# Kernel tuning notes

Hardware: AMD Instinct MI355X
Metric: run time of the kernel (lower is better)

Reference implementation:

```python
import jax, jax.numpy as jnp
import numpy as np

LEN_NOISE = 1000
LEN_INTERVAL_U = 50
INPUT_DIM = 3
OUTPUT_DIM = 3
HIDDEN_DIM = 512
LOGSIG_CH = INPUT_DIM + (INPUT_DIM * (INPUT_DIM - 1)) // 2  # depth-2 Lyndon basis: level1 + Levy area


def _static_schedule(window_size):
    """Replicates compute_multilevel_logsignature index logic + the u_logsigrnn
    pop-gating of the forward loop. All quantities are static given window_size."""
    tb = np.linspace(0.0, 1.0, LEN_NOISE)
    tu = tb[::LEN_INTERVAL_U]
    tt = np.linspace(0.0, 1.0, window_size)
    u_indices = np.searchsorted(tb, tu, side='right') - 1
    t_indices = np.searchsorted(tb, tt[1:], side='right') - 1
    u_idx_for_t = np.searchsorted(tu, tt[1:], side='right') - 1
    starts, ends, u_times, last = [], [], [], -1
    for it, iu in zip(t_indices, u_idx_for_t):
        iu = max(int(iu), 0)
        if iu != last:
            u_times.append(float(tu[iu]))
            last = iu
        starts.append(int(u_indices[iu]))
        ends.append(int(it))
    u_times.append(float(tt[-1]))
    gates, q = [], list(u_times)
    for t in tt:  # gate True -> last_h updated to h at this step
        if q and t >= q[0]:
            q.pop(0)
            gates.append(True)
        else:
            gates.append(False)
    return np.array(starts), np.array(ends), np.array(gates)


def _logsig_depth2(path, starts, ends):
    """Depth-2 log-signature (Lyndon basis) of path[:, starts[k]:ends[k]+1] with
    basepoint=True. Level-1 = endpoint (basepoint is 0); level-2 = Levy area,
    computed from a cumulative cross-product prefix sum (basepoint segment
    0 -> path[:,start] contributes zero area)."""
    cross = 0.5 * (path[:, :-1, :, None] * path[:, 1:, None, :]
                   - path[:, :-1, None, :] * path[:, 1:, :, None])  # [B,L-1,d,d]
    C = jnp.cumsum(cross, axis=1)
    C = jnp.concatenate([jnp.zeros_like(C[:, :1]), C], axis=1)      # [B,L,d,d]
    lvl1 = path[:, ends]                                            # [B,T-1,d]
    area = C[:, ends] - C[:, starts]                                # [B,T-1,d,d]
    iu, ju = np.triu_indices(path.shape[-1], k=1)
    return jnp.concatenate([lvl1, area[:, :, iu, ju]], axis=-1)     # [B,T-1,d+C(d,2)]


def setup_inputs() -> dict:
    key = jax.random.key(0)
    ks = jax.random.split(key, 8)
    B, W = 1024, 64
    in_rnn = HIDDEN_DIM + LOGSIG_CH

    def kaiming(k, shape):
        return jax.random.normal(k, shape, jnp.float32) * np.float32(np.sqrt(2.0 / shape[1]))

    return {
        "z": jax.random.normal(ks[0], (B, LEN_NOISE, INPUT_DIM), jnp.float32),
        "W1": kaiming(ks[1], (HIDDEN_DIM, in_rnn)),
        "b1": jnp.zeros((HIDDEN_DIM,), jnp.float32),
        "W2": kaiming(ks[2], (HIDDEN_DIM, HIDDEN_DIM)),
        "b2": jnp.zeros((HIDDEN_DIM,), jnp.float32),
        "W3": kaiming(ks[3], (HIDDEN_DIM, HIDDEN_DIM)),
        "b3": jnp.zeros((HIDDEN_DIM,), jnp.float32),
        "Wout": kaiming(ks[4], (OUTPUT_DIM, HIDDEN_DIM)),
        "batch_size": B,
        "window_size": W,
    }


def reference(z, W1, b1, W2, b2, W3, b3, Wout, batch_size, window_size):
    starts, ends, gates = _static_schedule(window_size)
    # Brownian path: z[:,0]=0, z[:,1:] *= sqrt(dt), cumsum
    dt = 1.0 / (LEN_NOISE - 1)
    zz = z.at[:, 0].set(0.0)
    zz = zz.at[:, 1:].multiply(np.float32(np.sqrt(dt)))
    bp = jnp.cumsum(zz, axis=1)                                     # [B,L,d]
    ls = _logsig_depth2(bp, starts, ends)                           # [B,T-1,ch]
    ls = jnp.concatenate([jnp.zeros_like(ls[:, :1]), ls], axis=1)   # [B,T,ch] (zero prepended)

    def mlp(x):  # FeedForwardNN([h,h]) + Tanh
        h = jax.nn.relu(x @ W1.T + b1)
        h = jax.nn.relu(h @ W2.T + b2)
        return jnp.tanh(h @ W3.T + b3)

    h0 = jnp.zeros((z.shape[0], HIDDEN_DIM), z.dtype)  # init_fixed=True

    def step(last_h, inp):
        ls_t, gate = inp
        h = mlp(jnp.concatenate([last_h, ls_t], axis=-1))
        out = h @ Wout.T  # linear, no bias
        return jnp.where(gate, h, last_h), out

    xs = (jnp.swapaxes(ls, 0, 1), jnp.asarray(gates))
    _, outs = jax.lax.scan(step, h0, xs)                            # [T,B,out]
    return jnp.swapaxes(outs, 0, 1)                                 # [B,T,out]
```

## Files before the change

kernel.cpp:

```cpp
#include <hip/hip_runtime.h>
#include <cmath>

#define WIN 64
#define HID 512
#define BATCH 1024
#define KIN 518

typedef _Float16 f16;
typedef _Float16 half8 __attribute__((ext_vector_type(8)));
typedef float f32x4 __attribute__((ext_vector_type(4)));
typedef unsigned short u16x4 __attribute__((ext_vector_type(4)));

struct Sched { int starts[63]; int ends[63]; };
struct TL { int t[8]; int gf[8]; };
struct Targ { int v[32]; };

__global__ __launch_bounds__(256)
void logsig_scan(const float* __restrict__ z, Sched sc,
                 ushort* __restrict__ lsh, float scale) {
  __shared__ float zs[3000];
  __shared__ float Cs[20][3];
  __shared__ float wtot[4][6];
  __shared__ float earr[63][6];
  __shared__ short fe_s[1000];
  const int tid = threadIdx.x;
  const int b = blockIdx.x;
  const int ln = tid & 63, wv = tid >> 6;

  const float4* zrow = (const float4*)(z + (size_t)b * 3000);
  for (int i = tid; i < 750; i += 256) ((float4*)zs)[i] = zrow[i];
  for (int i = tid; i < 1000; i += 256) fe_s[i] = -1;
  if (tid == 0) { Cs[0][0] = 0.f; Cs[0][1] = 0.f; Cs[0][2] = 0.f; }
  __syncthreads();
  if (tid < 63) fe_s[sc.ends[tid]] = (short)tid;
  __syncthreads();

  const int p0 = 4 * tid + 1;
  int myfe[4];
#pragma unroll
  for (int i = 0; i < 4; ++i) myfe[i] = (p0 + i <= 999) ? fe_s[p0 + i] : -1;

  float d0 = 0.f, d1 = 0.f, d2 = 0.f, A0 = 0.f, A1 = 0.f, A2 = 0.f;
  if (p0 <= 999) {
    float b0 = 0.f, b1 = 0.f, b2 = 0.f;
#pragma unroll
    for (int i = 0; i < 4; ++i) {
      int p = p0 + i;
      if (p > 999) break;
      float n0 = b0 + zs[p * 3 + 0] * scale;
      float n1 = b1 + zs[p * 3 + 1] * scale;
      float n2 = b2 + zs[p * 3 + 2] * scale;
      A0 += 0.5f * (b0 * n1 - b1 * n0);
      A1 += 0.5f * (b0 * n2 - b2 * n0);
      A2 += 0.5f * (b1 * n2 - b2 * n1);
      b0 = n0; b1 = n1; b2 = n2;
    }
    d0 = b0; d1 = b1; d2 = b2;
  }

#pragma unroll
  for (int off = 1; off < 64; off <<= 1) {
    float e0 = __shfl(d0, ln - off), e1 = __shfl(d1, ln - off), e2 = __shfl(d2, ln - off);
    float eA0 = __shfl(A0, ln - off), eA1 = __shfl(A1, ln - off), eA2 = __shfl(A2, ln - off);
    if (ln >= off) {
      A0 = eA0 + A0 + 0.5f * (e0 * d1 - e1 * d0);
      A1 = eA1 + A1 + 0.5f * (e0 * d2 - e2 * d0);
      A2 = eA2 + A2 + 0.5f * (e1 * d2 - e2 * d1);
      d0 += e0; d1 += e1; d2 += e2;
    }
  }
  if (ln == 63) {
    wtot[wv][0] = d0; wtot[wv][1] = d1; wtot[wv][2] = d2;
    wtot[wv][3] = A0; wtot[wv][4] = A1; wtot[wv][5] = A2;
  }
  __syncthreads();

  float P0 = 0.f, P1 = 0.f, P2 = 0.f, PA0 = 0.f, PA1 = 0.f, PA2 = 0.f;
  for (int w = 0; w < wv; ++w) {
    float t0 = wtot[w][0], t1 = wtot[w][1], t2 = wtot[w][2];
    PA0 = PA0 + wtot[w][3] + 0.5f * (P0 * t1 - P1 * t0);
    PA1 = PA1 + wtot[w][4] + 0.5f * (P0 * t2 - P2 * t0);
    PA2 = PA2 + wtot[w][5] + 0.5f * (P1 * t2 - P2 * t1);
    P0 += t0; P1 += t1; P2 += t2;
  }
  float L0 = __shfl(d0, ln - 1), L1 = __shfl(d1, ln - 1), L2 = __shfl(d2, ln - 1);
  float LA0 = __shfl(A0, ln - 1), LA1 = __shfl(A1, ln - 1), LA2 = __shfl(A2, ln - 1);
  if (ln == 0) { L0 = L1 = L2 = LA0 = LA1 = LA2 = 0.f; }
  float bp0 = P0 + L0, bp1 = P1 + L1, bp2 = P2 + L2;
  float C0 = PA0 + LA0 + 0.5f * (P0 * L1 - P1 * L0);
  float C1 = PA1 + LA1 + 0.5f * (P0 * L2 - P2 * L0);
  float C2 = PA2 + LA2 + 0.5f * (P1 * L2 - P2 * L1);

  if (p0 <= 999) {
#pragma unroll
    for (int i = 0; i < 4; ++i) {
      int p = p0 + i;
      if (p > 999) break;
      float n0 = bp0 + zs[p * 3 + 0] * scale;
      float n1 = bp1 + zs[p * 3 + 1] * scale;
      float n2 = bp2 + zs[p * 3 + 2] * scale;
      C0 += 0.5f * (bp0 * n1 - bp1 * n0);
      C1 += 0.5f * (bp0 * n2 - bp2 * n0);
      C2 += 0.5f * (bp1 * n2 - bp2 * n1);
      bp0 = n0; bp1 = n1; bp2 = n2;
      if (p % 50 == 0) {
        int s = p / 50;
        Cs[s][0] = C0; Cs[s][1] = C1; Cs[s][2] = C2;
      }
      int k = myfe[i];
      if (k >= 0) {
        earr[k][0] = bp0; earr[k][1] = bp1; earr[k][2] = bp2;
        earr[k][3] = C0;  earr[k][4] = C1;  earr[k][5] = C2;
      }
    }
  }
  __syncthreads();

  if (tid < 63) {
    int s = sc.starts[tid] / 50;
    half8 v = {};
    v[0] = (f16)earr[tid][0]; v[1] = (f16)earr[tid][1]; v[2] = (f16)earr[tid][2];
    v[3] = (f16)(earr[tid][3] - Cs[s][0]);
    v[4] = (f16)(earr[tid][4] - Cs[s][1]);
    v[5] = (f16)(earr[tid][5] - Cs[s][2]);
    half8 zz = {};
    half8* d = (half8*)(lsh + ((size_t)(tid + 1) * BATCH + b) * 64);
    d[0] = v;
#pragma unroll
    for (int q = 1; q < 8; ++q) d[q] = zz;
  } else if (tid == 63) {
    half8 zz = {};
    half8* d = (half8*)(lsh + (size_t)b * 64);
#pragma unroll
    for (int q = 0; q < 8; ++q) d[q] = zz;
  }
}

__global__ __launch_bounds__(256)
void cvt_all(const float* __restrict__ W1, const float* __restrict__ W2,
             const float* __restrict__ W3, ushort* __restrict__ W1h,
             ushort* __restrict__ W2h, ushort* __restrict__ W3h) {
  const int n1 = HID * (576 / 8);
  const int n2 = HID * (HID / 8);
  int i = blockIdx.x * 256 + threadIdx.x;
  const float* src; ushort* dst; int Ks, Kd;
  if (i < n1)           { src = W1; dst = W1h; Ks = KIN; Kd = 576; }
  else if (i < n1 + n2) { src = W2; dst = W2h; Ks = HID; Kd = HID; i -= n1; }
  else if (i < n1 + 2 * n2) { src = W3; dst = W3h; Ks = HID; Kd = HID; i -= n1 + n2; }
  else return;
  int nblk = Kd >> 3;
  int row = i / nblk, k = (i - row * nblk) * 8;
  half8 v;
#pragma unroll
  for (int j = 0; j < 8; ++j) {
    int kk = k + j;
    float f = (kk < Ks) ? src[(size_t)row * Ks + kk] : 0.f;
    v[j] = (f16)f;
  }
  *(half8*)&dst[(size_t)row * Kd + k] = v;
}

template<int FIRST>
__global__ __launch_bounds__(256)
void fused3(const ushort* __restrict__ carry, const ushort* __restrict__ lsh,
            TL tl,
            const ushort* __restrict__ W1h, const ushort* __restrict__ W2h,
            const ushort* __restrict__ W3h,
            const float* __restrict__ b1, const float* __restrict__ b2,
            const float* __restrict__ b3,
            ushort* __restrict__ act1, ushort* __restrict__ act2,
            ushort* __restrict__ Hall, int* flags, Targ tg) {
  __shared__ ushort lds[32768];
  char* ldsb = (char*)lds;
  const int tid = threadIdx.x;
  const int wv = tid >> 6, ln = tid & 63;
  const int slab = blockIdx.x;
  const int bn0 = blockIdx.y * 128;
  const int slot = slab >> 3;
  const int t = tl.t[slot], gated = tl.gf[slot];
  const int b0 = (slab & 7) * 128;
  const size_t gr0 = (size_t)slab * 128;
  const int xr0 = (wv >> 1) * 64, nr0 = (wv & 1) * 64;
  const int l15 = ln & 15, l4 = ln >> 4;
  const int targ = tg.v[slab];
  const ushort* lbase = lsh + (size_t)t * BATCH * 64;

  f32x4 acc[4][4];

  auto gemm = [&](auto xsrc, const ushort* W, int ldw, int k0, int nk) {
#pragma unroll
    for (int mi = 0; mi < 4; ++mi)
#pragma unroll
      for (int ni = 0; ni < 4; ++ni) acc[mi][ni] = (f32x4){0.f, 0.f, 0.f, 0.f};

    auto stage = [&](int bi, int kt) {
#pragma unroll
      for (int i = 0; i < 4; ++i) {
        int qq = (i * 4 + wv) * 64 + ln;
        int r = qq >> 3, sl = qq & 7, ss = sl ^ (r & 7);
        const ushort* src = xsrc(kt, r, ss);
        __builtin_amdgcn_global_load_lds(
            (const __attribute__((address_space(1))) unsigned int*)src,
            (__attribute__((address_space(3))) unsigned int*)
                (ldsb + bi * 32768 + (i * 4 + wv) * 1024), 16, 0, 0);
      }
#pragma unroll
      for (int i = 0; i < 4; ++i) {
        int qq = (i * 4 + wv) * 64 + ln;
        int r = qq >> 3, sl = qq & 7, ss = sl ^ (r & 7);
        const ushort* src = W + (size_t)(bn0 + r) * ldw + kt * 64 + ss * 8;
        __builtin_amdgcn_global_load_lds(
            (const __attribute__((address_space(1))) unsigned int*)src,
            (__attribute__((address_space(3))) unsigned int*)
                (ldsb + bi * 32768 + 16384 + (i * 4 + wv) * 1024), 16, 0, 0);
      }
    };

    stage(0, k0);
    int cur = 0;
    for (int kt = k0; kt < nk; ++kt) {
      if (kt + 1 < nk) {
        stage(cur ^ 1, kt + 1);
        asm volatile("s_waitcnt vmcnt(8)" ::: "memory");
      } else {
        asm volatile("s_waitcnt vmcnt(0)" ::: "memory");
      }
      __builtin_amdgcn_s_barrier();
      __builtin_amdgcn_sched_barrier(0);
#pragma unroll
      for (int kk = 0; kk < 2; ++kk) {
        half8 xf[4], wf[4];
#pragma unroll
        for (int mi = 0; mi < 4; ++mi) {
          int r = xr0 + mi * 16 + l15;
          int ss = (kk * 4 + l4) ^ (r & 7);
          xf[mi] = *(const half8*)(ldsb + cur * 32768 + r * 128 + ss * 16);
        }
#pragma unroll
        for (int ni = 0; ni < 4; ++ni) {
          int r = nr0 + ni * 16 + l15;
          int ss = (kk * 4 + l4) ^ (r & 7);
          wf[ni] = *(const half8*)(ldsb + cur * 32768 + 16384 + r * 128 + ss * 16);
        }
#pragma unroll
        for (int mi = 0; mi < 4; ++mi)
#pragma unroll
          for (int ni = 0; ni < 4; ++ni)
            acc[mi][ni] = __builtin_amdgcn_mfma_f32_16x16x32_f16(
                wf[ni], xf[mi], acc[mi][ni], 0, 0, 0);
      }
      __builtin_amdgcn_sched_barrier(0);
      asm volatile("s_waitcnt lgkmcnt(0)" ::: "memory");
      __builtin_amdgcn_s_barrier();
      cur ^= 1;
    }
  };

#define EPILOGUE(ACT, BIAS, STORE_STMT)                                       \
  do {                                                                        \
    _Pragma("unroll")                                                         \
    for (int mi = 0; mi < 4; ++mi) {                                          \
      _Pragma("unroll")                                                       \
      for (int ni = 0; ni < 4; ++ni) {                                        \
        int col = bn0 + nr0 + ni * 16 + l4 * 4;                               \
        float4 bv = *(const float4*)&(BIAS)[col];                             \
        float bb[4] = {bv.x, bv.y, bv.z, bv.w};                               \
        union { f16 h[4]; u16x4 u; } cv;                                      \
        _Pragma("unroll")                                                     \
        for (int j4 = 0; j4 < 4; ++j4) {                                      \
          float v = acc[mi][ni][j4] + bb[j4];                                 \
          if (ACT == 1) v = fmaxf(v, 0.f);                                    \
          else { float xc = fminf(fmaxf(v, -9.f), 9.f);                       \
                 float e = __expf(2.f * xc); v = (e - 1.f) / (e + 1.f); }     \
          cv.h[j4] = (f16)v;                                                  \
        }                                                                     \
        STORE_STMT;                                                           \
      }                                                                       \
    }                                                                         \
  } while (0)

#define SYNCSLAB(FI)                                                          \
  do {                                                                        \
    asm volatile("s_waitcnt vmcnt(0)" ::: "memory");                          \
    __syncthreads();                                                          \
    if (tid == 0) {                                                           \
      __hip_atomic_fetch_add(&flags[FI], 1, __ATOMIC_RELAXED,                 \
                             __HIP_MEMORY_SCOPE_AGENT);                       \
      while (__hip_atomic_load(&flags[FI], __ATOMIC_RELAXED,                  \
                               __HIP_MEMORY_SCOPE_AGENT) < targ)              \
        __builtin_amdgcn_s_sleep(2);                                          \
    }                                                                         \
    __syncthreads();                                                          \
  } while (0)

  if (FIRST) {
    gemm([&](int kt, int r, int ss) {
      (void)kt; return lbase + (size_t)(b0 + r) * 64 + ss * 8;
    }, W1h, 576, 8, 9);
  } else {
    gemm([&](int kt, int r, int ss) {
      int b_ = b0 + r;
      return (kt < 8) ? carry + (size_t)b_ * HID + kt * 64 + ss * 8
                      : lbase + (size_t)b_ * 64 + ss * 8;
    }, W1h, 576, 0, 9);
  }
  EPILOGUE(1, b1,
    *(u16x4*)&act1[(gr0 + xr0 + mi * 16 + l15) * 512 + col] = cv.u);
  SYNCSLAB(slab);

  gemm([&](int kt, int r, int ss) {
    return act1 + (gr0 + r) * (size_t)HID + kt * 64 + ss * 8;
  }, W2h, 512, 0, 8);
  EPILOGUE(1, b2,
    *(u16x4*)&act2[(gr0 + xr0 + mi * 16 + l15) * 512 + col] = cv.u);
  SYNCSLAB(64 + slab);

  gemm([&](int kt, int r, int ss) {
    return act2 + (gr0 + r) * (size_t)HID + kt * 64 + ss * 8;
  }, W3h, 512, 0, 8);
  EPILOGUE(2, b3,
    { size_t hrow = (size_t)t * BATCH + b0 + xr0 + mi * 16 + l15;
      u16x4* dst = (u16x4*)&Hall[hrow * 512 + col];
      if (gated) *dst = cv.u;
      else       __builtin_nontemporal_store(cv.u, dst); });
#undef EPILOGUE
#undef SYNCSLAB
}

__global__ __launch_bounds__(256)
void out_k(const ushort* __restrict__ Hall, const float* __restrict__ Wout,
           float* __restrict__ out) {
  const int tid = threadIdx.x;
  const int lane4 = tid & 3;
  const int row = blockIdx.x * 64 + (tid >> 2);
  const int t = row >> 10, b = row & 1023;
  const ushort* hb = Hall + (size_t)row * HID;
  float a0 = 0.f, a1 = 0.f, a2 = 0.f;
#pragma unroll 4
  for (int q = 0; q < 16; ++q) {
    int k = (q * 4 + lane4) * 8;
    half8 hv8 = *(const half8*)&hb[k];
#pragma unroll
    for (int j = 0; j < 8; ++j) {
      float h = (float)hv8[j];
      a0 += h * Wout[k + j];
      a1 += h * Wout[512 + k + j];
      a2 += h * Wout[1024 + k + j];
    }
  }
  a0 += __shfl_xor(a0, 1); a0 += __shfl_xor(a0, 2);
  a1 += __shfl_xor(a1, 1); a1 += __shfl_xor(a1, 2);
  a2 += __shfl_xor(a2, 1); a2 += __shfl_xor(a2, 2);
  if (lane4 == 0) {
    float* o = out + ((size_t)b * WIN + t) * 3;
    o[0] = a0; o[1] = a1; o[2] = a2;
  }
}

extern "C" void kernel_launch(void* const* d_in, const int* in_sizes, int n_in,
                              void* d_out, int out_size, void* d_ws, size_t ws_size,
                              hipStream_t stream) {
  (void)n_in; (void)out_size; (void)ws_size; (void)in_sizes;
  const float* z    = (const float*)d_in[0];
  const float* W1   = (const float*)d_in[1];
  const float* b1   = (const float*)d_in[2];
  const float* W2   = (const float*)d_in[3];
  const float* b2   = (const float*)d_in[4];
  const float* W3   = (const float*)d_in[5];
  const float* b3   = (const float*)d_in[6];
  const float* Wout = (const float*)d_in[7];
  float* out = (float*)d_out;

  double tb[1000], tt[64], tu[20];
  {
    double sb = 1.0 / 999.0; for (int i = 0; i < 1000; ++i) tb[i] = i * sb; tb[999] = 1.0;
    double st = 1.0 / 63.0;  for (int k = 0; k < 64; ++k)  tt[k] = k * st;  tt[63] = 1.0;
    for (int j = 0; j < 20; ++j) tu[j] = tb[50 * j];
  }
  auto ssr = [](const double* a, int n, double v) -> int {
    int lo = 0, hi = n;
    while (lo < hi) { int mid = (lo + hi) >> 1; if (a[mid] <= v) lo = mid + 1; else hi = mid; }
    return lo - 1;
  };
  Sched sc; int gates[64];
  {
    int u_indices[20];
    for (int j = 0; j < 20; ++j) u_indices[j] = ssr(tb, 1000, tu[j]);
    double u_times[80]; int nut = 0; int last = -1;
    for (int k = 1; k < 64; ++k) {
      int it = ssr(tb, 1000, tt[k]);
      int iu = ssr(tu, 20, tt[k]); if (iu < 0) iu = 0;
      if (iu != last) { u_times[nut++] = tu[iu]; last = iu; }
      sc.starts[k - 1] = u_indices[iu];
      sc.ends[k - 1] = it;
    }
    u_times[nut++] = tt[63];
    int qh = 0;
    for (int k = 0; k < 64; ++k) {
      if (qh < nut && tt[k] >= u_times[qh]) { ++qh; gates[k] = 1; } else gates[k] = 0;
    }
  }
  int seg[64], g[64], ng = 0, jlast = -1;
  for (int t = 0; t < WIN; ++t) {
    seg[t] = jlast;
    if (gates[t]) { g[ng] = t; jlast = ng; ++ng; }
  }

  char* p = (char*)d_ws;
  int* flags   = (int*)p;    p += 128 * 4;
  ushort* lsh  = (ushort*)p; p += (size_t)WIN * BATCH * 64 * 2;
  ushort* W1h  = (ushort*)p; p += (size_t)HID * 576 * 2;
  ushort* W2h  = (ushort*)p; p += (size_t)HID * HID * 2;
  ushort* W3h  = (ushort*)p; p += (size_t)HID * HID * 2;
  ushort* Hall = (ushort*)p; p += (size_t)WIN * BATCH * HID * 2;
  ushort* act1 = (ushort*)p; p += (size_t)4 * BATCH * HID * 2;
  ushort* act2 = (ushort*)p; p += (size_t)4 * BATCH * HID * 2;

  hipMemsetAsync(flags, 0, 128 * 4, stream);

  float scale = (float)std::sqrt(1.0 / 999.0);
  logsig_scan<<<BATCH, 256, 0, stream>>>(z, sc, lsh, scale);
  cvt_all<<<(HID * 72 + 2 * HID * 64 + 255) / 256, 256, 0, stream>>>(
      W1, W2, W3, W1h, W2h, W3h);

  Targ tg; for (int i = 0; i < 32; ++i) tg.v[i] = 0;
  for (int r = 0; r < ng; ++r) {
    TL tlr; int cnt = 0;
    for (int t = 0; t < WIN && cnt < 4; ++t)
      if (seg[t] == r - 1) tlr.t[cnt++] = t;
    if (cnt == 0) continue;
    for (int i = cnt; i < 8; ++i) tlr.t[i] = tlr.t[0];
    for (int i = 0; i < 8; ++i) tlr.gf[i] = (tlr.t[i] == g[r]) ? 1 : 0;
    for (int s = 0; s < cnt * 8; ++s) tg.v[s] += 4;
    const ushort* carry = (r == 0) ? nullptr : Hall + (size_t)g[r - 1] * (BATCH * HID);
    dim3 gg(cnt * 8, 4), gb(256);
    if (r == 0)
      fused3<1><<<gg, gb, 0, stream>>>(carry, lsh, tlr, W1h, W2h, W3h,
                                       b1, b2, b3, act1, act2, Hall, flags, tg);
    else
      fused3<0><<<gg, gb, 0, stream>>>(carry, lsh, tlr, W1h, W2h, W3h,
                                       b1, b2, b3, act1, act2, Hall, flags, tg);
  }

  out_k<<<WIN * BATCH / 64, 256, 0, stream>>>(Hall, Wout, out);
}
```

Before: 603.5 us.

## Fuse output projection into final GEMM epilogue and merge prep kernels

Computes the Wout projection inside the third-layer epilogue as per-block partial sums, reduced by a small out_sum kernel. Hidden states are now written to Hall only for gated steps. This removes the full 64x1024x512 half write and the separate out_k pass that re-read it. The logsig and weight-conversion kernels are merged into one launch. The cost is extra per-thread FMAs and shuffles in the epilogue plus an 8-way partial-sum buffer.

After: 614.5 us. About the same (+1.8%).

```diff
diff --git a/kernel.cpp b/kernel.cpp
--- a/kernel.cpp
+++ b/kernel.cpp
@@ -16,14 +16,38 @@
 struct Targ { int v[32]; };
 
 __global__ __launch_bounds__(256)
-void logsig_scan(const float* __restrict__ z, Sched sc,
-                 ushort* __restrict__ lsh, float scale) {
+void prep(const float* __restrict__ z, Sched sc, ushort* __restrict__ lsh,
+          float scale,
+          const float* __restrict__ W1, const float* __restrict__ W2,
+          const float* __restrict__ W3, ushort* __restrict__ W1h,
+          ushort* __restrict__ W2h, ushort* __restrict__ W3h) {
+  const int tid = threadIdx.x;
+  if (blockIdx.x >= 1024) {
+    const int n1 = HID * (576 / 8);
+    const int n2 = HID * (HID / 8);
+    int i = (blockIdx.x - 1024) * 256 + tid;
+    const float* src; ushort* dst; int Ks, Kd;
+    if (i < n1)                 { src = W1; dst = W1h; Ks = KIN; Kd = 576; }
+    else if (i < n1 + n2)       { src = W2; dst = W2h; Ks = HID; Kd = HID; i -= n1; }
+    else if (i < n1 + 2 * n2)   { src = W3; dst = W3h; Ks = HID; Kd = HID; i -= n1 + n2; }
+    else return;
+    int nblk = Kd >> 3;
+    int row = i / nblk, k = (i - row * nblk) * 8;
+    half8 v;
+#pragma unroll
+    for (int j = 0; j < 8; ++j) {
+      int kk = k + j;
+      float f = (kk < Ks) ? src[(size_t)row * Ks + kk] : 0.f;
+      v[j] = (f16)f;
+    }
+    *(half8*)&dst[(size_t)row * Kd + k] = v;
+    return;
+  }
   __shared__ float zs[3000];
   __shared__ float Cs[20][3];
   __shared__ float wtot[4][6];
   __shared__ float earr[63][6];
   __shared__ short fe_s[1000];
-  const int tid = threadIdx.x;
   const int b = blockIdx.x;
   const int ln = tid & 63, wv = tid >> 6;
 
@@ -136,30 +160,6 @@
   }
 }
 
-__global__ __launch_bounds__(256)
-void cvt_all(const float* __restrict__ W1, const float* __restrict__ W2,
-             const float* __restrict__ W3, ushort* __restrict__ W1h,
-             ushort* __restrict__ W2h, ushort* __restrict__ W3h) {
-  const int n1 = HID * (576 / 8);
-  const int n2 = HID * (HID / 8);
-  int i = blockIdx.x * 256 + threadIdx.x;
-  const float* src; ushort* dst; int Ks, Kd;
-  if (i < n1)           { src = W1; dst = W1h; Ks = KIN; Kd = 576; }
-  else if (i < n1 + n2) { src = W2; dst = W2h; Ks = HID; Kd = HID; i -= n1; }
-  else if (i < n1 + 2 * n2) { src = W3; dst = W3h; Ks = HID; Kd = HID; i -= n1 + n2; }
-  else return;
-  int nblk = Kd >> 3;
-  int row = i / nblk, k = (i - row * nblk) * 8;
-  half8 v;
-#pragma unroll
-  for (int j = 0; j < 8; ++j) {
-    int kk = k + j;
-    float f = (kk < Ks) ? src[(size_t)row * Ks + kk] : 0.f;
-    v[j] = (f16)f;
-  }
-  *(half8*)&dst[(size_t)row * Kd + k] = v;
-}
-
 template<int FIRST>
 __global__ __launch_bounds__(256)
 void fused3(const ushort* __restrict__ carry, const ushort* __restrict__ lsh,
@@ -168,8 +168,10 @@
             const ushort* __restrict__ W3h,
             const float* __restrict__ b1, const float* __restrict__ b2,
             const float* __restrict__ b3,
+            const float* __restrict__ Wout,
             ushort* __restrict__ act1, ushort* __restrict__ act2,
-            ushort* __restrict__ Hall, int* flags, Targ tg) {
+            ushort* __restrict__ Hall, float* __restrict__ outp,
+            int* flags, Targ tg) {
   __shared__ ushort lds[32768];
   char* ldsb = (char*)lds;
   const int tid = threadIdx.x;
@@ -270,8 +272,6 @@
         for (int j4 = 0; j4 < 4; ++j4) {                                      \
           float v = acc[mi][ni][j4] + bb[j4];                                 \
           if (ACT == 1) v = fmaxf(v, 0.f);                                    \
-          else { float xc = fminf(fmaxf(v, -9.f), 9.f);                       \
-                 float e = __expf(2.f * xc); v = (e - 1.f) / (e + 1.f); }     \
           cv.h[j4] = (f16)v;                                                  \
         }                                                                     \
         STORE_STMT;                                                           \
@@ -318,43 +318,72 @@
   gemm([&](int kt, int r, int ss) {
     return act2 + (gr0 + r) * (size_t)HID + kt * 64 + ss * 8;
   }, W3h, 512, 0, 8);
-  EPILOGUE(2, b3,
-    { size_t hrow = (size_t)t * BATCH + b0 + xr0 + mi * 16 + l15;
-      u16x4* dst = (u16x4*)&Hall[hrow * 512 + col];
-      if (gated) *dst = cv.u;
-      else       __builtin_nontemporal_store(cv.u, dst); });
+  {
+    float po[4][3];
+#pragma unroll
+    for (int mi = 0; mi < 4; ++mi) { po[mi][0] = 0.f; po[mi][1] = 0.f; po[mi][2] = 0.f; }
+#pragma unroll
+    for (int mi = 0; mi < 4; ++mi) {
+#pragma unroll
+      for (int ni = 0; ni < 4; ++ni) {
+        int col = bn0 + nr0 + ni * 16 + l4 * 4;
+        float4 bv = *(const float4*)&b3[col];
+        float4 w0 = *(const float4*)&Wout[col];
+        float4 w1 = *(const float4*)&Wout[512 + col];
+        float4 w2 = *(const float4*)&Wout[1024 + col];
+        float bb[4] = {bv.x, bv.y, bv.z, bv.w};
+        float W0[4] = {w0.x, w0.y, w0.z, w0.w};
+        float W1a[4] = {w1.x, w1.y, w1.z, w1.w};
+        float W2a[4] = {w2.x, w2.y, w2.z, w2.w};
+        union { f16 h[4]; u16x4 u; } cv;
+#pragma unroll
+        for (int j4 = 0; j4 < 4; ++j4) {
+          float v = acc[mi][ni][j4] + bb[j4];
+          float xc = fminf(fmaxf(v, -9.f), 9.f);
+          float e = __expf(2.f * xc); v = (e - 1.f) / (e + 1.f);
+          cv.h[j4] = (f16)v;
+          po[mi][0] += v * W0[j4];
+          po[mi][1] += v * W1a[j4];
+          po[mi][2] += v * W2a[j4];
+        }
+        if (gated) {
+          size_t hrow = (size_t)t * BATCH + b0 + xr0 + mi * 16 + l15;
+          *(u16x4*)&Hall[hrow * 512 + col] = cv.u;
+        }
+      }
+    }
+#pragma unroll
+    for (int mi = 0; mi < 4; ++mi) {
+#pragma unroll
+      for (int o = 0; o < 3; ++o) {
+        float s = po[mi][o];
+        s += __shfl_xor(s, 16);
+        s += __shfl_xor(s, 32);
+        po[mi][o] = s;
+      }
+      if (l4 == 0) {
+        int row = b0 + xr0 + mi * 16 + l15;
+        int y2 = blockIdx.y * 2 + (wv & 1);
+        float* op = outp + (((size_t)y2 * WIN + t) * BATCH + row) * 3;
+        op[0] = po[mi][0]; op[1] = po[mi][1]; op[2] = po[mi][2];
+      }
+    }
+  }
 #undef EPILOGUE
 #undef SYNCSLAB
 }
 
 __global__ __launch_bounds__(256)
-void out_k(const ushort* __restrict__ Hall, const float* __restrict__ Wout,
-           float* __restrict__ out) {
-  const int tid = threadIdx.x;
-  const int lane4 = tid & 3;
-  const int row = blockIdx.x * 64 + (tid >> 2);
-  const int t = row >> 10, b = row & 1023;
-  const ushort* hb = Hall + (size_t)row * HID;
-  float a0 = 0.f, a1 = 0.f, a2 = 0.f;
-#pragma unroll 4
-  for (int q = 0; q < 16; ++q) {
-    int k = (q * 4 + lane4) * 8;
-    half8 hv8 = *(const half8*)&hb[k];
-#pragma unroll
-    for (int j = 0; j < 8; ++j) {
-      float h = (float)hv8[j];
-      a0 += h * Wout[k + j];
-      a1 += h * Wout[512 + k + j];
-      a2 += h * Wout[1024 + k + j];
-    }
-  }
-  a0 += __shfl_xor(a0, 1); a0 += __shfl_xor(a0, 2);
-  a1 += __shfl_xor(a1, 1); a1 += __shfl_xor(a1, 2);
-  a2 += __shfl_xor(a2, 1); a2 += __shfl_xor(a2, 2);
-  if (lane4 == 0) {
-    float* o = out + ((size_t)b * WIN + t) * 3;
-    o[0] = a0; o[1] = a1; o[2] = a2;
-  }
+void out_sum(const float* __restrict__ outp, float* __restrict__ out) {
+  int idx = blockIdx.x * 256 + threadIdx.x;
+  if (idx >= BATCH * WIN * 3) return;
+  int o = idx % 3, bt = idx / 3;
+  int t = bt % WIN, b = bt / WIN;
+  float s = 0.f;
+#pragma unroll
+  for (int y = 0; y < 8; ++y)
+    s += outp[(((size_t)y * WIN + t) * BATCH + b) * 3 + o];
+  out[idx] = s;
 }
 
 extern "C" void kernel_launch(void* const* d_in, const int* in_sizes, int n_in,
@@ -415,13 +444,13 @@
   ushort* Hall = (ushort*)p; p += (size_t)WIN * BATCH * HID * 2;
   ushort* act1 = (ushort*)p; p += (size_t)4 * BATCH * HID * 2;
   ushort* act2 = (ushort*)p; p += (size_t)4 * BATCH * HID * 2;
+  float* outp  = (float*)p;  p += (size_t)8 * WIN * BATCH * 3 * 4;
 
   hipMemsetAsync(flags, 0, 128 * 4, stream);
 
   float scale = (float)std::sqrt(1.0 / 999.0);
-  logsig_scan<<<BATCH, 256, 0, stream>>>(z, sc, lsh, scale);
-  cvt_all<<<(HID * 72 + 2 * HID * 64 + 255) / 256, 256, 0, stream>>>(
-      W1, W2, W3, W1h, W2h, W3h);
+  prep<<<1024 + 400, 256, 0, stream>>>(z, sc, lsh, scale,
+                                       W1, W2, W3, W1h, W2h, W3h);
 
   Targ tg; for (int i = 0; i < 32; ++i) tg.v[i] = 0;
   for (int r = 0; r < ng; ++r) {
@@ -436,11 +465,13 @@
     dim3 gg(cnt * 8, 4), gb(256);
     if (r == 0)
       fused3<1><<<gg, gb, 0, stream>>>(carry, lsh, tlr, W1h, W2h, W3h,
-                                       b1, b2, b3, act1, act2, Hall, flags, tg);
+                                       b1, b2, b3, Wout, act1, act2, Hall,
+                                       outp, flags, tg);
     else
       fused3<0><<<gg, gb, 0, stream>>>(carry, lsh, tlr, W1h, W2h, W3h,
-                                       b1, b2, b3, act1, act2, Hall, flags, tg);
-  }
-
-  out_k<<<WIN * BATCH / 64, 256, 0, stream>>>(Hall, Wout, out);
+                                       b1, b2, b3, Wout, act1, act2, Hall,
+                                       outp, flags, tg);
+  }
+
+  out_sum<<<(BATCH * WIN * 3 + 255) / 256, 256, 0, stream>>>(outp, out);
 }
```
